# Optimization experiments

Hardware: AMD Instinct MI355X
Metric: run time of the kernel (lower is better)

Reference implementation:

```python
import jax, jax.numpy as jnp
import numpy as np

NUM_HEADS = 16
EPS = 1e-8


def _dyn_quant(x):
    # per-token symmetric int8 quantization (dynamic input scale)
    s = jnp.maximum(jnp.max(jnp.abs(x), axis=-1, keepdims=True) / 127.0, EPS)
    q = jnp.clip(jnp.round(x / s), -127.0, 127.0)
    return q, s


def _quant_weight(w):
    # per-output-channel symmetric int8 weight quantization; w: [out, in]
    s = jnp.maximum(jnp.max(jnp.abs(w), axis=1, keepdims=True) / 127.0, EPS)
    q = jnp.clip(jnp.round(w / s), -127.0, 127.0)
    return q, s


def _w8a8_linear(x, w, b):
    # W8A8 GEMM with int32-exact accumulation (values fit exactly in fp32),
    # dequantized by per-token input scale * per-channel weight scale.
    qx, sx = _dyn_quant(x)          # [B,N,C], [B,N,1]
    qw, sw = _quant_weight(w)       # [O,C],   [O,1]
    y = jnp.einsum('bnc,oc->bno', qx, qw) * (sx * sw[:, 0])
    return y + b


def setup_inputs() -> dict:
    key = jax.random.key(0)
    ks = jax.random.split(key, 9)
    B, N, L, C = 2, 4096, 512, 2048
    sc = 0.02  # realistic weight init scale
    return {
        'x':    jax.random.normal(ks[0], (B, N, C), jnp.float32),
        'cond': jax.random.normal(ks[1], (B, L, C), jnp.float32),
        'mask': jnp.zeros((B, N, L), jnp.float32),  # additive attention mask
        'wq': jax.random.normal(ks[2], (C, C), jnp.float32) * sc,
        'bq': jnp.zeros((C,), jnp.float32),
        'wk': jax.random.normal(ks[3], (C, C), jnp.float32) * sc,
        'bk': jnp.zeros((C,), jnp.float32),
        'wv': jax.random.normal(ks[4], (C, C), jnp.float32) * sc,
        'bv': jnp.zeros((C,), jnp.float32),
        'wo': jax.random.normal(ks[5], (C, C), jnp.float32) * sc,
        'bo': jnp.zeros((C,), jnp.float32),
    }


def reference(x, cond, mask, wq, bq, wk, bk, wv, bv, wo, bo):
    B, N, C = x.shape
    L = cond.shape[1]
    H = NUM_HEADS
    D = C // H
    inv_sqrt_d = np.float32(1.0 / np.sqrt(D))

    # quantized Q projection, fp K/V projections
    q = _w8a8_linear(x, wq, bq).reshape(B, N, H, D).transpose(0, 2, 1, 3)      # [B,H,N,D]
    k = (cond @ wk.T + bk).reshape(B, L, H, D).transpose(0, 2, 1, 3)           # [B,H,L,D]
    v = (cond @ wv.T + bv).reshape(B, L, H, D).transpose(0, 2, 1, 3)           # [B,H,L,D]

    # SDPA cross-attention with additive mask broadcast over heads
    scores = jnp.einsum('bhnd,bhld->bhnl', q, k) * inv_sqrt_d + mask[:, None]
    attn = jax.nn.softmax(scores, axis=-1)
    o = jnp.einsum('bhnl,bhld->bhnd', attn, v)
    o = o.transpose(0, 2, 1, 3).reshape(B, N, C)

    # fused quant_sum (per-token requant) + quantized output projection
    return _w8a8_linear(o, wo, bo)
```

## Files before the change

kernel.cpp:

```cpp
#include <hip/hip_runtime.h>
#include <cstdint>
#include <cstddef>


typedef __bf16 bf16;
typedef __bf16 bf16x8 __attribute__((ext_vector_type(8)));
typedef __bf16 bf16x4 __attribute__((ext_vector_type(4)));
typedef float  f32x4  __attribute__((ext_vector_type(4)));
typedef int    i32x4  __attribute__((ext_vector_type(4)));

#define DEV __device__ __forceinline__

static constexpr int CB = 2;
static constexpr int CN = 4096;
static constexpr int CL = 512;
static constexpr int CC = 2048;
static constexpr int CH = 16;
static constexpr int CD = 128;
static constexpr int TOK = CB * CN;
static constexpr int LR  = CB * CL;

DEV void gl_lds16(const void* g, void* l) {
  __builtin_amdgcn_global_load_lds(
      (const __attribute__((address_space(1))) unsigned int*)g,
      (__attribute__((address_space(3))) unsigned int*)l, 16, 0, 0);
}

DEV f32x4 mfma16(bf16x8 a, bf16x8 b, f32x4 c) {
  return __builtin_amdgcn_mfma_f32_16x16x32_bf16(a, b, c, 0, 0, 0);
}

DEV i32x4 mfma_i8(i32x4 a, i32x4 b, i32x4 c) {
  return __builtin_amdgcn_mfma_i32_16x16x64_i8(a, b, c, 0, 0, 0);
}

__global__ __launch_bounds__(256) void quant_rows_i8(
    const float* __restrict__ in, signed char* __restrict__ q,
    float* __restrict__ scale)
{
  const int r = blockIdx.x, t = threadIdx.x;
  const float* x = in + (size_t)r * CC;
  const float4 v0 = ((const float4*)x)[2 * t];
  const float4 v1 = ((const float4*)x)[2 * t + 1];
  float m = fmaxf(fmaxf(fmaxf(fabsf(v0.x), fabsf(v0.y)), fmaxf(fabsf(v0.z), fabsf(v0.w))),
                  fmaxf(fmaxf(fabsf(v1.x), fabsf(v1.y)), fmaxf(fabsf(v1.z), fabsf(v1.w))));
#pragma unroll
  for (int off = 32; off > 0; off >>= 1) m = fmaxf(m, __shfl_xor(m, off));
  __shared__ float sm[4];
  if ((t & 63) == 0) sm[t >> 6] = m;
  __syncthreads();
  m = fmaxf(fmaxf(sm[0], sm[1]), fmaxf(sm[2], sm[3]));
  const float s = fmaxf(m / 127.0f, 1e-8f);
  if (t == 0) scale[r] = s;
  const float a[8] = {v0.x, v0.y, v0.z, v0.w, v1.x, v1.y, v1.z, v1.w};
  int2 pk;
  int lo = 0, hi = 0;
#pragma unroll
  for (int j = 0; j < 4; j++) {
    const int b0 = (int)fminf(fmaxf(rintf(a[j]     / s), -127.f), 127.f);
    const int b1 = (int)fminf(fmaxf(rintf(a[4 + j] / s), -127.f), 127.f);
    lo |= (b0 & 255) << (8 * j);
    hi |= (b1 & 255) << (8 * j);
  }
  pk.x = lo; pk.y = hi;
  const int c0 = t * 8;
  const int f = (r >> 1) & 3;
  const int pos = (c0 & ~63) | ((((c0 >> 4) & 3) ^ f) << 4) | (c0 & 15);
  *(int2*)&q[(size_t)r * CC + pos] = pk;
}

__global__ __launch_bounds__(256) void split_pair_k(
    const float* __restrict__ in, bf16* __restrict__ hi, bf16* __restrict__ lo)
{
  const size_t i = (size_t)blockIdx.x * 256 + threadIdx.x;
  const float4 v = ((const float4*)in)[i];
  const float a[4] = {v.x, v.y, v.z, v.w};
  bf16x4 h4, l4;
#pragma unroll
  for (int j = 0; j < 4; j++) {
    bf16 h = (bf16)a[j];
    h4[j] = h;
    l4[j] = (bf16)(a[j] - (float)h);
  }
  ((bf16x4*)hi)[i] = h4;
  ((bf16x4*)lo)[i] = l4;
}

__global__ __launch_bounds__(256) void bias_split_k(
    const float* __restrict__ in, const float* __restrict__ bias,
    bf16* __restrict__ hi, bf16* __restrict__ lo)
{
  const size_t i = (size_t)blockIdx.x * 256 + threadIdx.x;
  const float4 v = ((const float4*)in)[i];
  const float4 bb = ((const float4*)bias)[i & (CC / 4 - 1)];
  const float a[4] = {v.x + bb.x, v.y + bb.y, v.z + bb.z, v.w + bb.w};
  bf16x4 h4, l4;
#pragma unroll
  for (int j = 0; j < 4; j++) {
    bf16 h = (bf16)a[j];
    h4[j] = h;
    l4[j] = (bf16)(a[j] - (float)h);
  }
  ((bf16x4*)hi)[i] = h4;
  ((bf16x4*)lo)[i] = l4;
}

__global__ __launch_bounds__(256) void bias_split_vt_k(
    const float* __restrict__ Vf, const float* __restrict__ bias,
    bf16* __restrict__ vth, bf16* __restrict__ vtl)
{
  __shared__ float tile[32][33];
  const int t = threadIdx.x;
  const int l0 = blockIdx.x * 32, d0 = blockIdx.y * 32, bh = blockIdx.z;
  const int b = bh >> 4, h = bh & 15;
  const int r = t >> 3, c4 = (t & 7) * 4;
  const float4 v = *(const float4*)&Vf[((size_t)b * CL + l0 + r) * CC + h * CD + d0 + c4];
  const float4 bb = *(const float4*)&bias[h * CD + d0 + c4];
  tile[r][c4 + 0] = v.x + bb.x;
  tile[r][c4 + 1] = v.y + bb.y;
  tile[r][c4 + 2] = v.z + bb.z;
  tile[r][c4 + 3] = v.w + bb.w;
  __syncthreads();
  bf16x4 h4, l4;
#pragma unroll
  for (int j = 0; j < 4; j++) {
    const float a = tile[c4 + j][r];
    const bf16 hh = (bf16)a;
    h4[j] = hh;
    l4[j] = (bf16)(a - (float)hh);
  }
  const size_t o = ((size_t)bh * CD + d0 + r) * CL + l0 + c4;
  *(bf16x4*)&vth[o] = h4;
  *(bf16x4*)&vtl[o] = l4;
}

template <int MODE>
__global__ __launch_bounds__(256) void gemm_i8(
    const signed char* __restrict__ A, const signed char* __restrict__ B,
    float* __restrict__ out0, bf16* __restrict__ outH, bf16* __restrict__ outL,
    const float* __restrict__ rowS, const float* __restrict__ colS,
    const float* __restrict__ bias, const int Nd, const int K)
{
  __shared__ signed char sA[2][128 * 64] __attribute__((aligned(16)));
  __shared__ signed char sB[2][128 * 64] __attribute__((aligned(16)));
  const int t = threadIdx.x;
  int lin = blockIdx.y * 16 + blockIdx.x;
  lin = (lin & 7) * 128 + (lin >> 3);
  const int m0 = (lin >> 4) * 128, n0 = (lin & 15) * 128;
  const int srow = t >> 2, scol = (t & 3) * 16;
  const signed char* aP = A + (size_t)(m0 + srow) * K + scol;
  const signed char* bP = B + (size_t)(n0 + srow) * K + scol;
  const int lane = t & 63, wave = t >> 6;
  const int wm = (wave >> 1) * 64, wn = (wave & 1) * 64;
  const int quad = lane >> 4, l16 = lane & 15;
  i32x4 acc[4][4] = {};

  gl_lds16(aP,                  &sA[0][t * 16]);
  gl_lds16(aP + (size_t)64 * K, &sA[0][4096 + t * 16]);
  gl_lds16(bP,                  &sB[0][t * 16]);
  gl_lds16(bP + (size_t)64 * K, &sB[0][4096 + t * 16]);
  __syncthreads();

  int cur = 0;
  for (int kb = 0; kb < K; kb += 64) {
    const int nx = kb + 64;
    if (nx < K) {
      gl_lds16(aP + nx,                  &sA[cur ^ 1][t * 16]);
      gl_lds16(aP + nx + (size_t)64 * K, &sA[cur ^ 1][4096 + t * 16]);
      gl_lds16(bP + nx,                  &sB[cur ^ 1][t * 16]);
      gl_lds16(bP + nx + (size_t)64 * K, &sB[cur ^ 1][4096 + t * 16]);
    }
    i32x4 fa[4], fb[4];
#pragma unroll
    for (int i = 0; i < 4; i++) {
      const int ra = wm + i * 16 + l16;
      const int rb = wn + i * 16 + l16;
      fa[i] = *(const i32x4*)&sA[cur][ra * 64 + (quad ^ ((ra >> 1) & 3)) * 16];
      fb[i] = *(const i32x4*)&sB[cur][rb * 64 + (quad ^ ((rb >> 1) & 3)) * 16];
    }
#pragma unroll
    for (int mt = 0; mt < 4; mt++)
#pragma unroll
      for (int nt = 0; nt < 4; nt++)
        acc[mt][nt] = mfma_i8(fa[mt], fb[nt], acc[mt][nt]);
    __syncthreads();
    cur ^= 1;
  }

#pragma unroll
  for (int mt = 0; mt < 4; mt++)
#pragma unroll
    for (int nt = 0; nt < 4; nt++)
#pragma unroll
      for (int rg = 0; rg < 4; rg++) {
        const int mr = m0 + wm + mt * 16 + quad * 4 + rg;
        const int nc = n0 + wn + nt * 16 + l16;
        const float a = (float)acc[mt][nt][rg];
        const float sc = rowS[mr] * colS[nc];
        const float v = a * sc + bias[nc];
        if (MODE == 0) {
          out0[(size_t)mr * Nd + nc] = v;
        } else {
          const bf16 h = (bf16)v;
          outH[(size_t)mr * Nd + nc] = h;
          outL[(size_t)mr * Nd + nc] = (bf16)(v - (float)h);
        }
      }
}

__global__ __launch_bounds__(256) void gemm_kv(
    const bf16* __restrict__ Ah, const bf16* __restrict__ Al,
    const bf16* __restrict__ B0h, const bf16* __restrict__ B0l,
    const bf16* __restrict__ B1h, const bf16* __restrict__ B1l,
    float* __restrict__ out0, float* __restrict__ out1,
    const int Nd, const int K, const int kLen)
{
  __shared__ bf16 sAh[128 * 32] __attribute__((aligned(16)));
  __shared__ bf16 sBh[128 * 32] __attribute__((aligned(16)));
  __shared__ bf16 sAl[128 * 32] __attribute__((aligned(16)));
  __shared__ bf16 sBl[128 * 32] __attribute__((aligned(16)));
  const int t = threadIdx.x;
  int lin = (blockIdx.z * 8 + blockIdx.y) * 16 + blockIdx.x;
  lin = (lin & 7) * 128 + (lin >> 3);
  const int bx = lin & 15, by = (lin >> 4) & 7, bz = lin >> 7;
  const int kv = bz >> 2, chunk = bz & 3;
  const bf16* Bh = kv ? B1h : B0h;
  const bf16* Bl = kv ? B1l : B0l;
  float* outF = kv ? out1 : out0;
  const int m0 = by * 128, n0 = bx * 128;
  const int k0 = chunk * kLen;
  const int srow = t >> 2, scol = (t & 3) * 8;
  const bf16* aP  = Ah + (size_t)(m0 + srow) * K + k0 + scol;
  const bf16* bP  = Bh + (size_t)(n0 + srow) * K + k0 + scol;
  const bf16* aPl = Al + (size_t)(m0 + srow) * K + k0 + scol;
  const bf16* bPl = Bl + (size_t)(n0 + srow) * K + k0 + scol;
  const int lane = t & 63, wave = t >> 6;
  const int wm = (wave >> 1) * 64, wn = (wave & 1) * 64;
  const int quad = lane >> 4, l16 = lane & 15;
  f32x4 acc[4][4] = {};

  for (int kb = 0; kb < kLen; kb += 32) {
    __syncthreads();
    gl_lds16(aP + kb,                   &sAh[t * 8]);
    gl_lds16(aP + kb + (size_t)64 * K,  &sAh[2048 + t * 8]);
    gl_lds16(bP + kb,                   &sBh[t * 8]);
    gl_lds16(bP + kb + (size_t)64 * K,  &sBh[2048 + t * 8]);
    gl_lds16(aPl + kb,                  &sAl[t * 8]);
    gl_lds16(aPl + kb + (size_t)64 * K, &sAl[2048 + t * 8]);
    gl_lds16(bPl + kb,                  &sBl[t * 8]);
    gl_lds16(bPl + kb + (size_t)64 * K, &sBl[2048 + t * 8]);
    __syncthreads();
    bf16x8 fa[4], fb[4], fal[4], fbl[4];
#pragma unroll
    for (int i = 0; i < 4; i++) {
      fa[i]  = *(const bf16x8*)&sAh[(wm + i * 16 + l16) * 32 + quad * 8];
      fb[i]  = *(const bf16x8*)&sBh[(wn + i * 16 + l16) * 32 + quad * 8];
      fal[i] = *(const bf16x8*)&sAl[(wm + i * 16 + l16) * 32 + quad * 8];
      fbl[i] = *(const bf16x8*)&sBl[(wn + i * 16 + l16) * 32 + quad * 8];
    }
#pragma unroll
    for (int mt = 0; mt < 4; mt++)
#pragma unroll
      for (int nt = 0; nt < 4; nt++) {
        f32x4 c = acc[mt][nt];
        c = mfma16(fa[mt],  fb[nt],  c);
        c = mfma16(fa[mt],  fbl[nt], c);
        c = mfma16(fal[mt], fb[nt],  c);
        acc[mt][nt] = c;
      }
  }

#pragma unroll
  for (int mt = 0; mt < 4; mt++)
#pragma unroll
    for (int nt = 0; nt < 4; nt++)
#pragma unroll
      for (int rg = 0; rg < 4; rg++) {
        const int mr = m0 + wm + mt * 16 + quad * 4 + rg;
        const int nc = n0 + wn + nt * 16 + l16;
        atomicAdd(&outF[(size_t)mr * Nd + nc], acc[mt][nt][rg]);
      }
}

__global__ __launch_bounds__(1024, 4) void attn_k(
    const bf16* __restrict__ qh, const bf16* __restrict__ ql,
    const bf16* __restrict__ kh, const bf16* __restrict__ kl,
    const bf16* __restrict__ vth, const bf16* __restrict__ vtl,
    const float* __restrict__ mask, float* __restrict__ O)
{
  __shared__ char arena[34816 + 32768 + 36864] __attribute__((aligned(16)));
  bf16 (*ksb)[2][32][136] = (bf16 (*)[2][32][136])arena;
  bf16 (*vtb)[2][128][32] = (bf16 (*)[2][128][32])(arena + 34816);
  float (*ps)[16][36] = (float (*)[16][36])(arena + 34816 + 32768);
  const int t = threadIdx.x, lane = t & 63, w = t >> 6;
  const int quad = lane >> 4, l16 = lane & 15;
  int lin = (blockIdx.z * 16 + blockIdx.y) * 16 + blockIdx.x;
  lin = (lin & 7) * 64 + (lin >> 3);
  const int n0 = (lin & 15) * 256;
  const int h  = (lin >> 4) & 15;
  const int b  = lin >> 8;
  const int bh = b * CH + h;
  const size_t qrow0 = (size_t)b * CN + n0;
  const float* mrow_base = mask + ((size_t)b * CN + n0 + w * 16 + quad * 4) * CL;

  const int pl   = t >> 9;
  const int krow = (t >> 4) & 31, ksg = t & 15;
  const int vrow = (t >> 2) & 127, vsg = t & 3;
  const bf16* kPsrc = pl ? kl : kh;
  const bf16* vPsrc = pl ? vtl : vth;
  const int vc = (vsg ^ ((vrow >> 3) & 3)) * 8;
  uint4 kr, vr;
  kr = *(const uint4*)(kPsrc + ((size_t)b * CL + krow) * CC + h * CD + ksg * 8);
  vr = *(const uint4*)(vPsrc + ((size_t)bh * CD + vrow) * CL + vsg * 8);

  bf16x8 qfh[4], qfl[4];
  {
    bf16* qs = (bf16*)arena;
    const int row = t >> 2, sg = t & 3;
    {
      const bf16* src = qh + (qrow0 + row) * CC + h * CD + sg * 32;
      bf16* dst = qs + row * 136 + sg * 32;
#pragma unroll
      for (int j = 0; j < 4; j++) ((uint4*)dst)[j] = ((const uint4*)src)[j];
    }
    __syncthreads();
#pragma unroll
    for (int s = 0; s < 4; s++)
      qfh[s] = *(const bf16x8*)&qs[(w * 16 + l16) * 136 + s * 32 + quad * 8];
    __syncthreads();
    {
      const bf16* src = ql + (qrow0 + row) * CC + h * CD + sg * 32;
      bf16* dst = qs + row * 136 + sg * 32;
#pragma unroll
      for (int j = 0; j < 4; j++) ((uint4*)dst)[j] = ((const uint4*)src)[j];
    }
    __syncthreads();
#pragma unroll
    for (int s = 0; s < 4; s++)
      qfl[s] = *(const bf16x8*)&qs[(w * 16 + l16) * 136 + s * 32 + quad * 8];
    __syncthreads();
  }

  *(uint4*)&ksb[0][pl][krow][ksg * 8] = kr;
  *(uint4*)&vtb[0][pl][vrow][vc] = vr;
  kr = *(const uint4*)(kPsrc + ((size_t)b * CL + 32 + krow) * CC + h * CD + ksg * 8);
  vr = *(const uint4*)(vPsrc + ((size_t)bh * CD + vrow) * CL + 32 + vsg * 8);

  f32x4 oacc[8] = {};
  f32x4 suma = {};
  const bf16 one = (bf16)1.0f;
  const bf16x8 ones = {one, one, one, one, one, one, one, one};
  const float isd = 0.08838834764831845f;

  for (int ci = 0; ci < CL / 32; ci++) {
    const int cur = ci & 1;
    __syncthreads();
    if (ci + 1 < CL / 32) {
      *(uint4*)&ksb[cur ^ 1][pl][krow][ksg * 8] = kr;
      *(uint4*)&vtb[cur ^ 1][pl][vrow][vc] = vr;
    }
    if (ci + 2 < CL / 32) {
      const int lcn = (ci + 2) * 32;
      kr = *(const uint4*)(kPsrc + ((size_t)b * CL + lcn + krow) * CC + h * CD + ksg * 8);
      vr = *(const uint4*)(vPsrc + ((size_t)bh * CD + vrow) * CL + lcn + vsg * 8);
    }
    const int lc = ci * 32;
    float mcur[2][4];
#pragma unroll
    for (int rg = 0; rg < 4; rg++) {
      const float* mrp = mrow_base + (size_t)rg * CL + lc;
      mcur[0][rg] = mrp[l16];
      mcur[1][rg] = mrp[16 + l16];
    }

    f32x4 sacc[2] = {};
    __builtin_amdgcn_s_setprio(1);
#pragma unroll
    for (int s = 0; s < 4; s++) {
#pragma unroll
      for (int lt = 0; lt < 2; lt++) {
        bf16x8 kbh = *(const bf16x8*)&ksb[cur][0][lt * 16 + l16][s * 32 + quad * 8];
        bf16x8 kbl = *(const bf16x8*)&ksb[cur][1][lt * 16 + l16][s * 32 + quad * 8];
        sacc[lt] = mfma16(qfh[s], kbh, sacc[lt]);
        sacc[lt] = mfma16(qfh[s], kbl, sacc[lt]);
        sacc[lt] = mfma16(qfl[s], kbh, sacc[lt]);
      }
    }
    __builtin_amdgcn_s_setprio(0);

    float u[2][4];
#pragma unroll
    for (int rg = 0; rg < 4; rg++) {
      u[0][rg] = __expf(sacc[0][rg] * isd + mcur[0][rg]);
      u[1][rg] = __expf(sacc[1][rg] * isd + mcur[1][rg]);
    }

#pragma unroll
    for (int lt = 0; lt < 2; lt++)
#pragma unroll
      for (int rg = 0; rg < 4; rg++)
        ps[w][quad * 4 + rg][lt * 16 + l16] = u[lt][rg];
    const float4 p0 = *(const float4*)&ps[w][l16][quad * 8];
    const float4 p1 = *(const float4*)&ps[w][l16][quad * 8 + 4];
    const float pv[8] = {p0.x, p0.y, p0.z, p0.w, p1.x, p1.y, p1.z, p1.w};
    bf16x8 ph, plv;
#pragma unroll
    for (int j = 0; j < 8; j++) {
      bf16 hh = (bf16)pv[j];
      ph[j] = hh;
      plv[j] = (bf16)(pv[j] - (float)hh);
    }

    suma = mfma16(ph, ones, suma);
    suma = mfma16(plv, ones, suma);
    __builtin_amdgcn_s_setprio(1);
#pragma unroll
    for (int nt = 0; nt < 8; nt++) {
      const int vrr = nt * 16 + l16;
      const int vsw = (quad ^ ((vrr >> 3) & 3)) * 8;
      bf16x8 vbh = *(const bf16x8*)&vtb[cur][0][vrr][vsw];
      bf16x8 vbl = *(const bf16x8*)&vtb[cur][1][vrr][vsw];
      f32x4 c = oacc[nt];
      c = mfma16(ph, vbh, c);
      c = mfma16(ph, vbl, c);
      c = mfma16(plv, vbh, c);
      oacc[nt] = c;
    }
    __builtin_amdgcn_s_setprio(0);
  }

  f32x4 inv;
#pragma unroll
  for (int rg = 0; rg < 4; rg++) inv[rg] = 1.0f / suma[rg];
#pragma unroll
  for (int nt = 0; nt < 8; nt++)
#pragma unroll
    for (int rg = 0; rg < 4; rg++) {
      const size_t row = qrow0 + w * 16 + quad * 4 + rg;
      O[row * CC + h * CD + nt * 16 + l16] = oacc[nt][rg] * inv[rg];
    }
}

extern "C" void kernel_launch(void* const* d_in, const int* in_sizes, int n_in,
                              void* d_out, int out_size, void* d_ws, size_t ws_size,
                              hipStream_t stream)
{
  (void)in_sizes; (void)n_in; (void)out_size; (void)ws_size;
  const float* x    = (const float*)d_in[0];
  const float* cond = (const float*)d_in[1];
  const float* mask = (const float*)d_in[2];
  const float* wq   = (const float*)d_in[3];
  const float* bq   = (const float*)d_in[4];
  const float* wk   = (const float*)d_in[5];
  const float* bk   = (const float*)d_in[6];
  const float* wv   = (const float*)d_in[7];
  const float* bv   = (const float*)d_in[8];
  const float* wo   = (const float*)d_in[9];
  const float* bo   = (const float*)d_in[10];
  float* out = (float*)d_out;

  char* wsb = (char*)d_ws;
  size_t off = 0;
  auto alloc = [&](size_t bytes) -> char* {
    char* p = wsb + off;
    off += (bytes + 255) & ~(size_t)255;
    return p;
  };
  signed char* qx  = (signed char*)alloc((size_t)TOK * CC);
  signed char* qwq = (signed char*)alloc((size_t)CC * CC);
  bf16* ch  = (bf16*)alloc((size_t)LR * CC * 2);
  bf16* cl_ = (bf16*)alloc((size_t)LR * CC * 2);
  bf16* wkh = (bf16*)alloc((size_t)CC * CC * 2);
  bf16* wkl = (bf16*)alloc((size_t)CC * CC * 2);
  bf16* wvh = (bf16*)alloc((size_t)CC * CC * 2);
  bf16* wvl = (bf16*)alloc((size_t)CC * CC * 2);
  float* Kf = (float*)alloc((size_t)LR * CC * 4);
  float* Vf = (float*)alloc((size_t)LR * CC * 4);
  float* Obuf = (float*)qx;
  bf16* qhb = (bf16*)alloc((size_t)TOK * CC * 2);
  bf16* qlb = (bf16*)alloc((size_t)TOK * CC * 2);
  bf16* khb = (bf16*)alloc((size_t)LR * CC * 2);
  bf16* klb = (bf16*)alloc((size_t)LR * CC * 2);
  bf16* vth = (bf16*)alloc((size_t)LR * CC * 2);
  bf16* vtl = (bf16*)alloc((size_t)LR * CC * 2);
  signed char* qwo = (signed char*)alloc((size_t)CC * CC);
  float* sx  = (float*)alloc((size_t)TOK * 4);
  float* swq = (float*)alloc((size_t)CC * 4);
  float* swo = (float*)alloc((size_t)CC * 4);
  float* sO  = (float*)alloc((size_t)TOK * 4);
  signed char* qO = (signed char*)qhb;

  quant_rows_i8<<<CC,  256, 0, stream>>>(wq, qwq, swq);
  quant_rows_i8<<<CC,  256, 0, stream>>>(wo, qwo, swo);
  quant_rows_i8<<<TOK, 256, 0, stream>>>(x, qx, sx);
  split_pair_k<<<(LR * CC / 4) / 256, 256, 0, stream>>>(cond, ch, cl_);
  split_pair_k<<<(CC * CC / 4) / 256, 256, 0, stream>>>(wk, wkh, wkl);
  split_pair_k<<<(CC * CC / 4) / 256, 256, 0, stream>>>(wv, wvh, wvl);
  gemm_i8<1><<<dim3(CC / 128, TOK / 128, 1), 256, 0, stream>>>(
      qx, qwq, nullptr, qhb, qlb, sx, swq, bq, CC, CC);
  (void)hipMemsetAsync(Kf, 0, (size_t)LR * CC * 4 * 2, stream);
  gemm_kv<<<dim3(CC / 128, LR / 128, 8), 256, 0, stream>>>(
      ch, cl_, wkh, wkl, wvh, wvl, Kf, Vf, CC, CC, 512);
  bias_split_k<<<(LR * CC / 4) / 256, 256, 0, stream>>>(Kf, bk, khb, klb);
  bias_split_vt_k<<<dim3(CL / 32, CD / 32, CB * CH), 256, 0, stream>>>(Vf, bv, vth, vtl);
  attn_k<<<dim3(CN / 256, CH, CB), 1024, 0, stream>>>(
      qhb, qlb, khb, klb, vth, vtl, mask, Obuf);
  quant_rows_i8<<<TOK, 256, 0, stream>>>(Obuf, qO, sO);
  gemm_i8<0><<<dim3(CC / 128, TOK / 128, 1), 256, 0, stream>>>(
      qO, qwo, out, nullptr, nullptr, sO, swo, bo, CC, CC);
}
```

Baseline: 553.9 us.

## Fuse K/V projection with bias, hi/lo split and V transpose, dropping split-K atomics

Replaces the split-K K/V GEMM, which used atomicAdd into fp32 buffers plus a memset and two separate bias/split/transpose kernels, with a single full-K GEMM. It double-buffers the LDS tiles and applies the bias, the bf16 hi/lo split and the V transpose in its epilogue. This removes the fp32 K/V round trip, the atomics and three launches. The cost is a grid of 256 blocks instead of 1024, so parallelism drops, and each block now runs a loop four times longer.

```diff
diff --git a/kernel.cpp b/kernel.cpp
--- a/kernel.cpp
+++ b/kernel.cpp
@@ -84,54 +84,6 @@
   }
   ((bf16x4*)hi)[i] = h4;
   ((bf16x4*)lo)[i] = l4;
-}
-
-__global__ __launch_bounds__(256) void bias_split_k(
-    const float* __restrict__ in, const float* __restrict__ bias,
-    bf16* __restrict__ hi, bf16* __restrict__ lo)
-{
-  const size_t i = (size_t)blockIdx.x * 256 + threadIdx.x;
-  const float4 v = ((const float4*)in)[i];
-  const float4 bb = ((const float4*)bias)[i & (CC / 4 - 1)];
-  const float a[4] = {v.x + bb.x, v.y + bb.y, v.z + bb.z, v.w + bb.w};
-  bf16x4 h4, l4;
-#pragma unroll
-  for (int j = 0; j < 4; j++) {
-    bf16 h = (bf16)a[j];
-    h4[j] = h;
-    l4[j] = (bf16)(a[j] - (float)h);
-  }
-  ((bf16x4*)hi)[i] = h4;
-  ((bf16x4*)lo)[i] = l4;
-}
-
-__global__ __launch_bounds__(256) void bias_split_vt_k(
-    const float* __restrict__ Vf, const float* __restrict__ bias,
-    bf16* __restrict__ vth, bf16* __restrict__ vtl)
-{
-  __shared__ float tile[32][33];
-  const int t = threadIdx.x;
-  const int l0 = blockIdx.x * 32, d0 = blockIdx.y * 32, bh = blockIdx.z;
-  const int b = bh >> 4, h = bh & 15;
-  const int r = t >> 3, c4 = (t & 7) * 4;
-  const float4 v = *(const float4*)&Vf[((size_t)b * CL + l0 + r) * CC + h * CD + d0 + c4];
-  const float4 bb = *(const float4*)&bias[h * CD + d0 + c4];
-  tile[r][c4 + 0] = v.x + bb.x;
-  tile[r][c4 + 1] = v.y + bb.y;
-  tile[r][c4 + 2] = v.z + bb.z;
-  tile[r][c4 + 3] = v.w + bb.w;
-  __syncthreads();
-  bf16x4 h4, l4;
-#pragma unroll
-  for (int j = 0; j < 4; j++) {
-    const float a = tile[c4 + j][r];
-    const bf16 hh = (bf16)a;
-    h4[j] = hh;
-    l4[j] = (bf16)(a - (float)hh);
-  }
-  const size_t o = ((size_t)bh * CD + d0 + r) * CL + l0 + c4;
-  *(bf16x4*)&vth[o] = h4;
-  *(bf16x4*)&vtl[o] = l4;
 }
 
 template <int MODE>
@@ -208,55 +160,68 @@
       }
 }
 
-__global__ __launch_bounds__(256) void gemm_kv(
+__global__ __launch_bounds__(256) void gemm_kv2(
     const bf16* __restrict__ Ah, const bf16* __restrict__ Al,
     const bf16* __restrict__ B0h, const bf16* __restrict__ B0l,
     const bf16* __restrict__ B1h, const bf16* __restrict__ B1l,
-    float* __restrict__ out0, float* __restrict__ out1,
-    const int Nd, const int K, const int kLen)
+    bf16* __restrict__ outKh, bf16* __restrict__ outKl,
+    bf16* __restrict__ outVh, bf16* __restrict__ outVl,
+    const float* __restrict__ bk, const float* __restrict__ bv)
 {
-  __shared__ bf16 sAh[128 * 32] __attribute__((aligned(16)));
-  __shared__ bf16 sBh[128 * 32] __attribute__((aligned(16)));
-  __shared__ bf16 sAl[128 * 32] __attribute__((aligned(16)));
-  __shared__ bf16 sBl[128 * 32] __attribute__((aligned(16)));
+  __shared__ char arena[128 * 129 * 4] __attribute__((aligned(16)));
+  bf16 (*sAh)[128 * 32] = (bf16 (*)[128 * 32])(arena);
+  bf16 (*sBh)[128 * 32] = (bf16 (*)[128 * 32])(arena + 16384);
+  bf16 (*sAl)[128 * 32] = (bf16 (*)[128 * 32])(arena + 32768);
+  bf16 (*sBl)[128 * 32] = (bf16 (*)[128 * 32])(arena + 49152);
   const int t = threadIdx.x;
+  const int K = CC;
   int lin = (blockIdx.z * 8 + blockIdx.y) * 16 + blockIdx.x;
-  lin = (lin & 7) * 128 + (lin >> 3);
-  const int bx = lin & 15, by = (lin >> 4) & 7, bz = lin >> 7;
-  const int kv = bz >> 2, chunk = bz & 3;
+  lin = (lin & 7) * 32 + (lin >> 3);
+  const int n0 = (lin & 15) * 128;
+  const int m0 = ((lin >> 4) & 7) * 128;
+  const int kv = lin >> 7;
   const bf16* Bh = kv ? B1h : B0h;
   const bf16* Bl = kv ? B1l : B0l;
-  float* outF = kv ? out1 : out0;
-  const int m0 = by * 128, n0 = bx * 128;
-  const int k0 = chunk * kLen;
   const int srow = t >> 2, scol = (t & 3) * 8;
-  const bf16* aP  = Ah + (size_t)(m0 + srow) * K + k0 + scol;
-  const bf16* bP  = Bh + (size_t)(n0 + srow) * K + k0 + scol;
-  const bf16* aPl = Al + (size_t)(m0 + srow) * K + k0 + scol;
-  const bf16* bPl = Bl + (size_t)(n0 + srow) * K + k0 + scol;
+  const bf16* aP  = Ah + (size_t)(m0 + srow) * K + scol;
+  const bf16* bP  = Bh + (size_t)(n0 + srow) * K + scol;
+  const bf16* aPl = Al + (size_t)(m0 + srow) * K + scol;
+  const bf16* bPl = Bl + (size_t)(n0 + srow) * K + scol;
   const int lane = t & 63, wave = t >> 6;
   const int wm = (wave >> 1) * 64, wn = (wave & 1) * 64;
   const int quad = lane >> 4, l16 = lane & 15;
   f32x4 acc[4][4] = {};
 
-  for (int kb = 0; kb < kLen; kb += 32) {
-    __syncthreads();
-    gl_lds16(aP + kb,                   &sAh[t * 8]);
-    gl_lds16(aP + kb + (size_t)64 * K,  &sAh[2048 + t * 8]);
-    gl_lds16(bP + kb,                   &sBh[t * 8]);
-    gl_lds16(bP + kb + (size_t)64 * K,  &sBh[2048 + t * 8]);
-    gl_lds16(aPl + kb,                  &sAl[t * 8]);
-    gl_lds16(aPl + kb + (size_t)64 * K, &sAl[2048 + t * 8]);
-    gl_lds16(bPl + kb,                  &sBl[t * 8]);
-    gl_lds16(bPl + kb + (size_t)64 * K, &sBl[2048 + t * 8]);
-    __syncthreads();
+  gl_lds16(aP,                  &sAh[0][t * 8]);
+  gl_lds16(aP + (size_t)64 * K, &sAh[0][2048 + t * 8]);
+  gl_lds16(bP,                  &sBh[0][t * 8]);
+  gl_lds16(bP + (size_t)64 * K, &sBh[0][2048 + t * 8]);
+  gl_lds16(aPl,                  &sAl[0][t * 8]);
+  gl_lds16(aPl + (size_t)64 * K, &sAl[0][2048 + t * 8]);
+  gl_lds16(bPl,                  &sBl[0][t * 8]);
+  gl_lds16(bPl + (size_t)64 * K, &sBl[0][2048 + t * 8]);
+  __syncthreads();
+
+  int cur = 0;
+  for (int kb = 0; kb < K; kb += 32) {
+    const int nx = kb + 32;
+    if (nx < K) {
+      gl_lds16(aP + nx,                  &sAh[cur ^ 1][t * 8]);
+      gl_lds16(aP + nx + (size_t)64 * K, &sAh[cur ^ 1][2048 + t * 8]);
+      gl_lds16(bP + nx,                  &sBh[cur ^ 1][t * 8]);
+      gl_lds16(bP + nx + (size_t)64 * K, &sBh[cur ^ 1][2048 + t * 8]);
+      gl_lds16(aPl + nx,                  &sAl[cur ^ 1][t * 8]);
+      gl_lds16(aPl + nx + (size_t)64 * K, &sAl[cur ^ 1][2048 + t * 8]);
+      gl_lds16(bPl + nx,                  &sBl[cur ^ 1][t * 8]);
+      gl_lds16(bPl + nx + (size_t)64 * K, &sBl[cur ^ 1][2048 + t * 8]);
+    }
     bf16x8 fa[4], fb[4], fal[4], fbl[4];
 #pragma unroll
     for (int i = 0; i < 4; i++) {
-      fa[i]  = *(const bf16x8*)&sAh[(wm + i * 16 + l16) * 32 + quad * 8];
-      fb[i]  = *(const bf16x8*)&sBh[(wn + i * 16 + l16) * 32 + quad * 8];
-      fal[i] = *(const bf16x8*)&sAl[(wm + i * 16 + l16) * 32 + quad * 8];
-      fbl[i] = *(const bf16x8*)&sBl[(wn + i * 16 + l16) * 32 + quad * 8];
+      fa[i]  = *(const bf16x8*)&sAh[cur][(wm + i * 16 + l16) * 32 + quad * 8];
+      fb[i]  = *(const bf16x8*)&sBh[cur][(wn + i * 16 + l16) * 32 + quad * 8];
+      fal[i] = *(const bf16x8*)&sAl[cur][(wm + i * 16 + l16) * 32 + quad * 8];
+      fbl[i] = *(const bf16x8*)&sBl[cur][(wn + i * 16 + l16) * 32 + quad * 8];
     }
 #pragma unroll
     for (int mt = 0; mt < 4; mt++)
@@ -268,18 +233,54 @@
         c = mfma16(fal[mt], fb[nt],  c);
         acc[mt][nt] = c;
       }
-  }
-
-#pragma unroll
-  for (int mt = 0; mt < 4; mt++)
-#pragma unroll
-    for (int nt = 0; nt < 4; nt++)
-#pragma unroll
-      for (int rg = 0; rg < 4; rg++) {
-        const int mr = m0 + wm + mt * 16 + quad * 4 + rg;
-        const int nc = n0 + wn + nt * 16 + l16;
-        atomicAdd(&outF[(size_t)mr * Nd + nc], acc[mt][nt][rg]);
+    __syncthreads();
+    cur ^= 1;
+  }
+
+  if (kv == 0) {
+#pragma unroll
+    for (int mt = 0; mt < 4; mt++)
+#pragma unroll
+      for (int nt = 0; nt < 4; nt++)
+#pragma unroll
+        for (int rg = 0; rg < 4; rg++) {
+          const int mr = m0 + wm + mt * 16 + quad * 4 + rg;
+          const int nc = n0 + wn + nt * 16 + l16;
+          const float v = acc[mt][nt][rg] + bk[nc];
+          const bf16 h = (bf16)v;
+          outKh[(size_t)mr * CC + nc] = h;
+          outKl[(size_t)mr * CC + nc] = (bf16)(v - (float)h);
+        }
+  } else {
+    float (*tile)[129] = (float (*)[129])arena;
+#pragma unroll
+    for (int mt = 0; mt < 4; mt++)
+#pragma unroll
+      for (int nt = 0; nt < 4; nt++)
+#pragma unroll
+        for (int rg = 0; rg < 4; rg++) {
+          const int lm = wm + mt * 16 + quad * 4 + rg;
+          const int ln = wn + nt * 16 + l16;
+          tile[lm][ln] = acc[mt][nt][rg] + bv[n0 + ln];
+        }
+    __syncthreads();
+    const int h = n0 >> 7, b = m0 >> 9, lbase = m0 & (CL - 1);
+    const int d = t & 127, half = t >> 7;
+    const size_t orow = ((size_t)(b * CH + h) * CD + d) * CL + lbase + half * 64;
+#pragma unroll
+    for (int jv = 0; jv < 8; jv++) {
+      bf16x8 h8, l8;
+#pragma unroll
+      for (int j = 0; j < 8; j++) {
+        const float v = tile[half * 64 + jv * 8 + j][d];
+        const bf16 hh = (bf16)v;
+        h8[j] = hh;
+        l8[j] = (bf16)(v - (float)hh);
       }
+      *(bf16x8*)&outVh[orow + jv * 8] = h8;
+      *(bf16x8*)&outVl[orow + jv * 8] = l8;
+    }
+  }
 }
 
 __global__ __launch_bounds__(1024, 4) void attn_k(
@@ -474,8 +475,7 @@
   bf16* wkl = (bf16*)alloc((size_t)CC * CC * 2);
   bf16* wvh = (bf16*)alloc((size_t)CC * CC * 2);
   bf16* wvl = (bf16*)alloc((size_t)CC * CC * 2);
-  float* Kf = (float*)alloc((size_t)LR * CC * 4);
-  float* Vf = (float*)alloc((size_t)LR * CC * 4);
+  (void)alloc((size_t)16 << 20);
   float* Obuf = (float*)qx;
   bf16* qhb = (bf16*)alloc((size_t)TOK * CC * 2);
   bf16* qlb = (bf16*)alloc((size_t)TOK * CC * 2);
@@ -498,11 +498,8 @@
   split_pair_k<<<(CC * CC / 4) / 256, 256, 0, stream>>>(wv, wvh, wvl);
   gemm_i8<1><<<dim3(CC / 128, TOK / 128, 1), 256, 0, stream>>>(
       qx, qwq, nullptr, qhb, qlb, sx, swq, bq, CC, CC);
-  (void)hipMemsetAsync(Kf, 0, (size_t)LR * CC * 4 * 2, stream);
-  gemm_kv<<<dim3(CC / 128, LR / 128, 8), 256, 0, stream>>>(
-      ch, cl_, wkh, wkl, wvh, wvl, Kf, Vf, CC, CC, 512);
-  bias_split_k<<<(LR * CC / 4) / 256, 256, 0, stream>>>(Kf, bk, khb, klb);
-  bias_split_vt_k<<<dim3(CL / 32, CD / 32, CB * CH), 256, 0, stream>>>(Vf, bv, vth, vtl);
+  gemm_kv2<<<dim3(CC / 128, LR / 128, 2), 256, 0, stream>>>(
+      ch, cl_, wkh, wkl, wvh, wvl, khb, klb, vth, vtl, bk, bv);
   attn_k<<<dim3(CN / 256, CH, CB), 1024, 0, stream>>>(
       qhb, qlb, khb, klb, vth, vtl, mask, Obuf);
   quant_rows_i8<<<TOK, 256, 0, stream>>>(Obuf, qO, sO);
```

After: 500.5 us. 9.7% less time.
